# Kernel tuning notes

Hardware: AMD Instinct MI355X
Metric: run time of the kernel (lower is better)

## Reference

```python
import jax, jax.numpy as jnp
from jax import lax
import numpy as np

S, B, I, H = 1024, 512, 5, 32
G = 4 * H  # torch LSTM gate dim, order: i, f, g, o


def setup_inputs() -> dict:
    key = jax.random.key(0)
    ks = jax.random.split(key, 19)
    n = lambda k, shape, s=0.1: jax.random.normal(k, shape, jnp.float32) * s
    return {
        "x": jax.random.normal(ks[0], (S, B, I), jnp.float32),
        "Wih0": n(ks[1], (G, I)), "Whh0": n(ks[2], (G, H)), "bih0": n(ks[3], (G,)), "bhh0": n(ks[4], (G,)),
        "Wih1": n(ks[5], (G, H)), "Whh1": n(ks[6], (G, H)), "bih1": n(ks[7], (G,)), "bhh1": n(ks[8], (G,)),
        "Wih2": n(ks[9], (G, H)), "Whh2": n(ks[10], (G, H)), "bih2": n(ks[11], (G,)), "bhh2": n(ks[12], (G,)),
        "w1": n(ks[13], (H, H)), "b1": n(ks[14], (H,)),
        "w2": n(ks[15], (H, H)), "b2": n(ks[16], (H,)),
        "w3": n(ks[17], (1, H)), "b3": n(ks[18], (1,)),
    }


def lstm_layer(x, Wih, Whh, bih, bhh):
    # x: [S, B, in]; precompute input projections for all steps (one big GEMM)
    xp = jnp.einsum("sbi,gi->sbg", x, Wih) + bih + bhh  # [S, B, 4H]
    h0 = jnp.zeros((x.shape[1], H), x.dtype)
    c0 = jnp.zeros((x.shape[1], H), x.dtype)

    def step(carry, xg):
        h, c = carry
        gates = xg + h @ Whh.T  # [B, 4H]
        i, f, g, o = jnp.split(gates, 4, axis=-1)
        c = jax.nn.sigmoid(f) * c + jax.nn.sigmoid(i) * jnp.tanh(g)
        h = jax.nn.sigmoid(o) * jnp.tanh(c)
        return (h, c), h

    _, ys = lax.scan(step, (h0, c0), xp)
    return ys  # [S, B, H]


def reference(x, Wih0, Whh0, bih0, bhh0, Wih1, Whh1, bih1, bhh1,
              Wih2, Whh2, bih2, bhh2, w1, b1, w2, b2, w3, b3):
    h = lstm_layer(x, Wih0, Whh0, bih0, bhh0)
    h = lstm_layer(h, Wih1, Whh1, bih1, bhh1)
    h = lstm_layer(h, Wih2, Whh2, bih2, bhh2)  # [S, B, H]
    s, b, hd = h.shape
    y = h.reshape(s * b, hd)
    y = y @ w1.T + b1
    y = y @ w2.T + b2
    y = y @ w3.T + b3
    y = jax.nn.relu(y)
    return y.reshape(s, b, -1)  # [S, B, 1]
```

## Files before the change

kernel.cpp:

```cpp
#include <hip/hip_runtime.h>
#include <math.h>

#define S_LEN 1024
#define BATCH 512
#define HID   32

#define LOG2E 1.44269504088896340736f

__device__ __forceinline__ float fast_rcp(float x) { return __builtin_amdgcn_rcpf(x); }
__device__ __forceinline__ float fast_exp2(float x) { return __builtin_amdgcn_exp2f(x); }

__device__ __forceinline__ void tick_barrier() {
    asm volatile("s_waitcnt lgkmcnt(0)" ::: "memory");
    __builtin_amdgcn_s_barrier();
    asm volatile("" ::: "memory");
}

typedef unsigned int uint2v __attribute__((ext_vector_type(2)));
__device__ __forceinline__ void swap_halves(float v, float& hiAll, float& loAll) {
    uint2v r = __builtin_amdgcn_permlane32_swap(__float_as_uint(v),
                                                __float_as_uint(v),
                                                false, false);
    hiAll = __uint_as_float(r[0]);
    loAll = __uint_as_float(r[1]);
}

__device__ __forceinline__ float bcast(float v, int k) {
    return __int_as_float(__builtin_amdgcn_readlane(__float_as_int(v), k));
}

#define LOADROW(dst, base, row, sc)                                            \
    {                                                                          \
        const float4* W_ = reinterpret_cast<const float4*>((base) +            \
                                                    (size_t)(row) * HID);      \
        _Pragma("unroll")                                                      \
        for (int k4 = 0; k4 < 8; ++k4) {                                       \
            float4 v_ = W_[k4];                                                \
            dst[4 * k4 + 0] = v_.x * (sc);                                     \
            dst[4 * k4 + 1] = v_.y * (sc);                                     \
            dst[4 * k4 + 2] = v_.z * (sc);                                     \
            dst[4 * k4 + 3] = v_.w * (sc);                                     \
        }                                                                      \
    }

__global__ __launch_bounds__(192)
__attribute__((amdgpu_waves_per_eu(1, 2)))
void lstm3_fused(const float* __restrict__ x,
                 const float* __restrict__ Wih0, const float* __restrict__ Whh0,
                 const float* __restrict__ bih0, const float* __restrict__ bhh0,
                 const float* __restrict__ Wih1, const float* __restrict__ Whh1,
                 const float* __restrict__ bih1, const float* __restrict__ bhh1,
                 const float* __restrict__ Wih2, const float* __restrict__ Whh2,
                 const float* __restrict__ bih2, const float* __restrict__ bhh2,
                 float* __restrict__ hseq)
{
    const int b = blockIdx.x;
    const int w = threadIdx.x >> 6;
    const int l = threadIdx.x & 63;
    const int j = l & 31;
    const bool lowHalf = (l < 32);
    const int gA = l;
    const int gB = l + 64;
    const float sA = LOG2E;
    const float sB = lowHalf ? (2.0f * LOG2E) : LOG2E;

    __shared__ float4 xl4[S_LEN];
    __shared__ float  xl1[S_LEN];
    __shared__ float ring[2][2][HID];

    for (int i = threadIdx.x; i < 2 * 2 * HID; i += 192)
        (&ring[0][0][0])[i] = 0.0f;
    {
        float* xf = reinterpret_cast<float*>(xl4);
        for (int idx = threadIdx.x; idx < S_LEN * 5; idx += 192) {
            const int s = idx / 5;
            const int c = idx - 5 * s;
            const float v = x[(size_t)s * (BATCH * 5) + b * 5 + c];
            if (c < 4) xf[s * 4 + c] = v;
            else       xl1[s] = v;
        }
    }

    const float* Wih = (w == 0) ? Wih0 : (w == 1) ? Wih1 : Wih2;
    const float* Whh = (w == 0) ? Whh0 : (w == 1) ? Whh1 : Whh2;
    const float* bih = (w == 0) ? bih0 : (w == 1) ? bih1 : bih2;
    const float* bhh = (w == 0) ? bhh0 : (w == 1) ? bhh1 : bhh2;

    float whA[HID], whB[HID];
    LOADROW(whA, Whh, gA, sA);
    LOADROW(whB, Whh, gB, sB);
    float wiA[HID], wiB[HID];
    float wxA[5], wxB[5];
    if (w == 0) {
#pragma unroll
        for (int k = 0; k < 5; ++k) {
            wxA[k] = Wih[gA * 5 + k] * sA;
            wxB[k] = Wih[gB * 5 + k] * sB;
        }
    } else {
        LOADROW(wiA, Wih, gA, sA);
        LOADROW(wiB, Wih, gB, sB);
    }
    const float biasA = (bih[gA] + bhh[gA]) * sA;
    const float biasB = (bih[gB] + bhh[gB]) * sB;

    float c = 0.0f;
    float h_own = 0.0f;

    __syncthreads();

    for (int t = 0; t < S_LEN + 2; ++t) {
        const int s = t - w;
        const bool active = (s >= 0) && (s < S_LEN);
        const int p = t & 1;

        float aA0 = biasA, aA1 = 0.f, aA2 = 0.f, aA3 = 0.f;
        float aB0 = biasB, aB1 = 0.f, aB2 = 0.f, aB3 = 0.f;

#pragma unroll
        for (int k4 = 0; k4 < HID / 4; ++k4) {
            const float h0 = bcast(h_own, 4 * k4 + 0);
            const float h1 = bcast(h_own, 4 * k4 + 1);
            const float h2 = bcast(h_own, 4 * k4 + 2);
            const float h3 = bcast(h_own, 4 * k4 + 3);
            aA0 += whA[4 * k4 + 0] * h0;
            aA1 += whA[4 * k4 + 1] * h1;
            aA2 += whA[4 * k4 + 2] * h2;
            aA3 += whA[4 * k4 + 3] * h3;
            aB0 += whB[4 * k4 + 0] * h0;
            aB1 += whB[4 * k4 + 1] * h1;
            aB2 += whB[4 * k4 + 2] * h2;
            aB3 += whB[4 * k4 + 3] * h3;
        }

        if (w == 0) {
            if (active) {
                const float4 xv = xl4[s];
                const float  x4 = xl1[s];
                aA0 += wxA[0] * xv.x; aB0 += wxB[0] * xv.x;
                aA1 += wxA[1] * xv.y; aB1 += wxB[1] * xv.y;
                aA2 += wxA[2] * xv.z; aB2 += wxB[2] * xv.z;
                aA3 += wxA[3] * xv.w; aB3 += wxB[3] * xv.w;
                aA0 += wxA[4] * x4;   aB0 += wxB[4] * x4;
            }
        } else {
            const float4* hin4 = reinterpret_cast<const float4*>(&ring[p][w - 1][0]);
#pragma unroll
            for (int k4 = 0; k4 < HID / 4; ++k4) {
                float4 hv = hin4[k4];
                aA0 += wiA[4 * k4 + 0] * hv.x;
                aA1 += wiA[4 * k4 + 1] * hv.y;
                aA2 += wiA[4 * k4 + 2] * hv.z;
                aA3 += wiA[4 * k4 + 3] * hv.w;
                aB0 += wiB[4 * k4 + 0] * hv.x;
                aB1 += wiB[4 * k4 + 1] * hv.y;
                aB2 += wiB[4 * k4 + 2] * hv.z;
                aB3 += wiB[4 * k4 + 3] * hv.w;
            }
        }
        const float accA = (aA0 + aA1) + (aA2 + aA3);
        const float accB = (aB0 + aB1) + (aB2 + aB3);

        float yf, yi, yo, yg;
        swap_halves(accA, yf, yi);
        swap_halves(accB, yo, yg);

        const float gi = fast_rcp(1.0f + fast_exp2(-yi));
        const float gf = fast_rcp(1.0f + fast_exp2(-yf));
        const float sg = fast_rcp(1.0f + fast_exp2(-yg));
        const float go = fast_rcp(1.0f + fast_exp2(-yo));
        const float gg = 2.0f * sg - 1.0f;

        const float c_new = gf * c + gi * gg;
        const float e  = fast_exp2(-2.0f * LOG2E * fabsf(c_new));
        const float tc = copysignf((1.0f - e) * fast_rcp(1.0f + e), c_new);
        const float h = go * tc;

        if (active) {
            c = c_new;
            h_own = h;
            if (w < 2) {
                if (lowHalf) ring[p ^ 1][w][j] = h;
            } else {
                if (lowHalf)
                    hseq[((size_t)s * BATCH + b) * HID + j] = h;
            }
        }
        tick_barrier();
    }
}

__global__ __launch_bounds__(256)
void mlp_kernel(const float* __restrict__ h, const float* __restrict__ w1,
                const float* __restrict__ b1, const float* __restrict__ w2,
                const float* __restrict__ b2, const float* __restrict__ w3,
                const float* __restrict__ b3, float* __restrict__ out)
{
    __shared__ float W1[HID * HID];
    __shared__ float W2[HID * HID];
    __shared__ float W3[HID];
    __shared__ float B1[HID];
    __shared__ float B2[HID];
    __shared__ float B3s;

    for (int i = threadIdx.x; i < HID * HID; i += blockDim.x) {
        W1[i] = w1[i];
        W2[i] = w2[i];
    }
    if (threadIdx.x < HID) {
        W3[threadIdx.x] = w3[threadIdx.x];
        B1[threadIdx.x] = b1[threadIdx.x];
        B2[threadIdx.x] = b2[threadIdx.x];
    }
    if (threadIdx.x == 0) B3s = b3[0];
    __syncthreads();

    const size_t e = (size_t)blockIdx.x * blockDim.x + threadIdx.x;
    float hv[HID];
    const float4* hp = reinterpret_cast<const float4*>(h + e * HID);
#pragma unroll
    for (int k4 = 0; k4 < HID / 4; ++k4) {
        float4 v = hp[k4];
        hv[4 * k4 + 0] = v.x;
        hv[4 * k4 + 1] = v.y;
        hv[4 * k4 + 2] = v.z;
        hv[4 * k4 + 3] = v.w;
    }

    float y1[HID];
#pragma unroll
    for (int jj = 0; jj < HID; ++jj) {
        float acc = B1[jj];
#pragma unroll
        for (int k = 0; k < HID; ++k) acc += W1[jj * HID + k] * hv[k];
        y1[jj] = acc;
    }
    float y2[HID];
#pragma unroll
    for (int jj = 0; jj < HID; ++jj) {
        float acc = B2[jj];
#pragma unroll
        for (int k = 0; k < HID; ++k) acc += W2[jj * HID + k] * y1[k];
        y2[jj] = acc;
    }
    float acc3 = B3s;
#pragma unroll
    for (int k = 0; k < HID; ++k) acc3 += W3[k] * y2[k];
    out[e] = fmaxf(acc3, 0.0f);
}

extern "C" void kernel_launch(void* const* d_in, const int* in_sizes, int n_in,
                              void* d_out, int out_size, void* d_ws, size_t ws_size,
                              hipStream_t stream)
{
    const float* x    = (const float*)d_in[0];
    const float* Wih0 = (const float*)d_in[1];
    const float* Whh0 = (const float*)d_in[2];
    const float* bih0 = (const float*)d_in[3];
    const float* bhh0 = (const float*)d_in[4];
    const float* Wih1 = (const float*)d_in[5];
    const float* Whh1 = (const float*)d_in[6];
    const float* bih1 = (const float*)d_in[7];
    const float* bhh1 = (const float*)d_in[8];
    const float* Wih2 = (const float*)d_in[9];
    const float* Whh2 = (const float*)d_in[10];
    const float* bih2 = (const float*)d_in[11];
    const float* bhh2 = (const float*)d_in[12];
    const float* w1   = (const float*)d_in[13];
    const float* b1   = (const float*)d_in[14];
    const float* w2   = (const float*)d_in[15];
    const float* b2   = (const float*)d_in[16];
    const float* w3   = (const float*)d_in[17];
    const float* b3   = (const float*)d_in[18];

    float* hseq = (float*)d_ws;

    lstm3_fused<<<BATCH, 192, 0, stream>>>(x, Wih0, Whh0, bih0, bhh0,
                                           Wih1, Whh1, bih1, bhh1,
                                           Wih2, Whh2, bih2, bhh2, hseq);

    mlp_kernel<<<(S_LEN * BATCH) / 256, 256, 0, stream>>>(hseq, w1, b1, w2, b2, w3, b3,
                                                          (float*)d_out);
}
```

Before: 888.4 us.

## Process two batch elements per block to reuse register-resident weights

Each block now handles two batch columns instead of one, so the recurrent and input weight rows held in registers serve two independent LSTM chains, and the launch uses half as many blocks. The two chains interleave inside each timestep, which gives more instruction-level parallelism per wave and halves the number of per-step barriers counted across the whole grid. The costs are twice the LDS for the staged inputs and ring buffers, more accumulator registers, and only 256 blocks, which may underfill the GPU and lengthen the serial path each block walks.

```diff
diff --git a/kernel.cpp b/kernel.cpp
--- a/kernel.cpp
+++ b/kernel.cpp
@@ -4,6 +4,7 @@
 #define S_LEN 1024
 #define BATCH 512
 #define HID   32
+#define BPB   2
 
 #define LOG2E 1.44269504088896340736f
 
@@ -54,7 +55,7 @@
                  const float* __restrict__ bih2, const float* __restrict__ bhh2,
                  float* __restrict__ hseq)
 {
-    const int b = blockIdx.x;
+    const int b0 = blockIdx.x * BPB;
     const int w = threadIdx.x >> 6;
     const int l = threadIdx.x & 63;
     const int j = l & 31;
@@ -64,20 +65,21 @@
     const float sA = LOG2E;
     const float sB = lowHalf ? (2.0f * LOG2E) : LOG2E;
 
-    __shared__ float4 xl4[S_LEN];
-    __shared__ float  xl1[S_LEN];
-    __shared__ float ring[2][2][HID];
-
-    for (int i = threadIdx.x; i < 2 * 2 * HID; i += 192)
-        (&ring[0][0][0])[i] = 0.0f;
+    __shared__ float4 xl4[BPB][S_LEN];
+    __shared__ float  xl1[BPB][S_LEN];
+    __shared__ float ring[2][2][BPB][HID];
+
+    for (int i = threadIdx.x; i < 2 * 2 * BPB * HID; i += 192)
+        (&ring[0][0][0][0])[i] = 0.0f;
     {
-        float* xf = reinterpret_cast<float*>(xl4);
-        for (int idx = threadIdx.x; idx < S_LEN * 5; idx += 192) {
-            const int s = idx / 5;
-            const int c = idx - 5 * s;
-            const float v = x[(size_t)s * (BATCH * 5) + b * 5 + c];
-            if (c < 4) xf[s * 4 + c] = v;
-            else       xl1[s] = v;
+        for (int idx = threadIdx.x; idx < BPB * S_LEN * 5; idx += 192) {
+            const int bb = idx / (S_LEN * 5);
+            const int r  = idx - bb * (S_LEN * 5);
+            const int s  = r / 5;
+            const int c  = r - 5 * s;
+            const float v = x[(size_t)s * (BATCH * 5) + (b0 + bb) * 5 + c];
+            if (c < 4) reinterpret_cast<float*>(&xl4[bb][0])[s * 4 + c] = v;
+            else       xl1[bb][s] = v;
         }
     }
 
@@ -104,8 +106,8 @@
     const float biasA = (bih[gA] + bhh[gA]) * sA;
     const float biasB = (bih[gB] + bhh[gB]) * sB;
 
-    float c = 0.0f;
-    float h_own = 0.0f;
+    float cst[BPB]  = {0.0f, 0.0f};
+    float hown[BPB] = {0.0f, 0.0f};
 
     __syncthreads();
 
@@ -114,76 +116,93 @@
         const bool active = (s >= 0) && (s < S_LEN);
         const int p = t & 1;
 
-        float aA0 = biasA, aA1 = 0.f, aA2 = 0.f, aA3 = 0.f;
-        float aB0 = biasB, aB1 = 0.f, aB2 = 0.f, aB3 = 0.f;
+        float aA[BPB][4], aB[BPB][4];
+#pragma unroll
+        for (int bb = 0; bb < BPB; ++bb) {
+            aA[bb][0] = biasA; aA[bb][1] = 0.f; aA[bb][2] = 0.f; aA[bb][3] = 0.f;
+            aB[bb][0] = biasB; aB[bb][1] = 0.f; aB[bb][2] = 0.f; aB[bb][3] = 0.f;
+        }
 
 #pragma unroll
         for (int k4 = 0; k4 < HID / 4; ++k4) {
-            const float h0 = bcast(h_own, 4 * k4 + 0);
-            const float h1 = bcast(h_own, 4 * k4 + 1);
-            const float h2 = bcast(h_own, 4 * k4 + 2);
-            const float h3 = bcast(h_own, 4 * k4 + 3);
-            aA0 += whA[4 * k4 + 0] * h0;
-            aA1 += whA[4 * k4 + 1] * h1;
-            aA2 += whA[4 * k4 + 2] * h2;
-            aA3 += whA[4 * k4 + 3] * h3;
-            aB0 += whB[4 * k4 + 0] * h0;
-            aB1 += whB[4 * k4 + 1] * h1;
-            aB2 += whB[4 * k4 + 2] * h2;
-            aB3 += whB[4 * k4 + 3] * h3;
+#pragma unroll
+            for (int bb = 0; bb < BPB; ++bb) {
+                const float h0 = bcast(hown[bb], 4 * k4 + 0);
+                const float h1 = bcast(hown[bb], 4 * k4 + 1);
+                const float h2 = bcast(hown[bb], 4 * k4 + 2);
+                const float h3 = bcast(hown[bb], 4 * k4 + 3);
+                aA[bb][0] += whA[4 * k4 + 0] * h0;
+                aA[bb][1] += whA[4 * k4 + 1] * h1;
+                aA[bb][2] += whA[4 * k4 + 2] * h2;
+                aA[bb][3] += whA[4 * k4 + 3] * h3;
+                aB[bb][0] += whB[4 * k4 + 0] * h0;
+                aB[bb][1] += whB[4 * k4 + 1] * h1;
+                aB[bb][2] += whB[4 * k4 + 2] * h2;
+                aB[bb][3] += whB[4 * k4 + 3] * h3;
+            }
         }
 
         if (w == 0) {
             if (active) {
-                const float4 xv = xl4[s];
-                const float  x4 = xl1[s];
-                aA0 += wxA[0] * xv.x; aB0 += wxB[0] * xv.x;
-                aA1 += wxA[1] * xv.y; aB1 += wxB[1] * xv.y;
-                aA2 += wxA[2] * xv.z; aB2 += wxB[2] * xv.z;
-                aA3 += wxA[3] * xv.w; aB3 += wxB[3] * xv.w;
-                aA0 += wxA[4] * x4;   aB0 += wxB[4] * x4;
+#pragma unroll
+                for (int bb = 0; bb < BPB; ++bb) {
+                    const float4 xv = xl4[bb][s];
+                    const float  x4 = xl1[bb][s];
+                    aA[bb][0] += wxA[0] * xv.x; aB[bb][0] += wxB[0] * xv.x;
+                    aA[bb][1] += wxA[1] * xv.y; aB[bb][1] += wxB[1] * xv.y;
+                    aA[bb][2] += wxA[2] * xv.z; aB[bb][2] += wxB[2] * xv.z;
+                    aA[bb][3] += wxA[3] * xv.w; aB[bb][3] += wxB[3] * xv.w;
+                    aA[bb][0] += wxA[4] * x4;   aB[bb][0] += wxB[4] * x4;
+                }
             }
         } else {
-            const float4* hin4 = reinterpret_cast<const float4*>(&ring[p][w - 1][0]);
 #pragma unroll
             for (int k4 = 0; k4 < HID / 4; ++k4) {
-                float4 hv = hin4[k4];
-                aA0 += wiA[4 * k4 + 0] * hv.x;
-                aA1 += wiA[4 * k4 + 1] * hv.y;
-                aA2 += wiA[4 * k4 + 2] * hv.z;
-                aA3 += wiA[4 * k4 + 3] * hv.w;
-                aB0 += wiB[4 * k4 + 0] * hv.x;
-                aB1 += wiB[4 * k4 + 1] * hv.y;
-                aB2 += wiB[4 * k4 + 2] * hv.z;
-                aB3 += wiB[4 * k4 + 3] * hv.w;
+#pragma unroll
+                for (int bb = 0; bb < BPB; ++bb) {
+                    const float4 hv = reinterpret_cast<const float4*>(
+                                          &ring[p][w - 1][bb][0])[k4];
+                    aA[bb][0] += wiA[4 * k4 + 0] * hv.x;
+                    aA[bb][1] += wiA[4 * k4 + 1] * hv.y;
+                    aA[bb][2] += wiA[4 * k4 + 2] * hv.z;
+                    aA[bb][3] += wiA[4 * k4 + 3] * hv.w;
+                    aB[bb][0] += wiB[4 * k4 + 0] * hv.x;
+                    aB[bb][1] += wiB[4 * k4 + 1] * hv.y;
+                    aB[bb][2] += wiB[4 * k4 + 2] * hv.z;
+                    aB[bb][3] += wiB[4 * k4 + 3] * hv.w;
+                }
             }
         }
-        const float accA = (aA0 + aA1) + (aA2 + aA3);
-        const float accB = (aB0 + aB1) + (aB2 + aB3);
-
-        float yf, yi, yo, yg;
-        swap_halves(accA, yf, yi);
-        swap_halves(accB, yo, yg);
-
-        const float gi = fast_rcp(1.0f + fast_exp2(-yi));
-        const float gf = fast_rcp(1.0f + fast_exp2(-yf));
-        const float sg = fast_rcp(1.0f + fast_exp2(-yg));
-        const float go = fast_rcp(1.0f + fast_exp2(-yo));
-        const float gg = 2.0f * sg - 1.0f;
-
-        const float c_new = gf * c + gi * gg;
-        const float e  = fast_exp2(-2.0f * LOG2E * fabsf(c_new));
-        const float tc = copysignf((1.0f - e) * fast_rcp(1.0f + e), c_new);
-        const float h = go * tc;
-
-        if (active) {
-            c = c_new;
-            h_own = h;
-            if (w < 2) {
-                if (lowHalf) ring[p ^ 1][w][j] = h;
-            } else {
-                if (lowHalf)
-                    hseq[((size_t)s * BATCH + b) * HID + j] = h;
+
+#pragma unroll
+        for (int bb = 0; bb < BPB; ++bb) {
+            const float accA = (aA[bb][0] + aA[bb][1]) + (aA[bb][2] + aA[bb][3]);
+            const float accB = (aB[bb][0] + aB[bb][1]) + (aB[bb][2] + aB[bb][3]);
+
+            float yf, yi, yo, yg;
+            swap_halves(accA, yf, yi);
+            swap_halves(accB, yo, yg);
+
+            const float gi = fast_rcp(1.0f + fast_exp2(-yi));
+            const float gf = fast_rcp(1.0f + fast_exp2(-yf));
+            const float sg = fast_rcp(1.0f + fast_exp2(-yg));
+            const float go = fast_rcp(1.0f + fast_exp2(-yo));
+            const float gg = 2.0f * sg - 1.0f;
+
+            const float c_new = gf * cst[bb] + gi * gg;
+            const float e  = fast_exp2(-2.0f * LOG2E * fabsf(c_new));
+            const float tc = copysignf((1.0f - e) * fast_rcp(1.0f + e), c_new);
+            const float h = go * tc;
+
+            if (active) {
+                cst[bb] = c_new;
+                hown[bb] = h;
+                if (w < 2) {
+                    if (lowHalf) ring[p ^ 1][w][bb][j] = h;
+                } else {
+                    if (lowHalf)
+                        hseq[((size_t)s * BATCH + (b0 + bb)) * HID + j] = h;
+                }
             }
         }
         tick_barrier();
@@ -275,9 +294,9 @@
 
     float* hseq = (float*)d_ws;
 
-    lstm3_fused<<<BATCH, 192, 0, stream>>>(x, Wih0, Whh0, bih0, bhh0,
-                                           Wih1, Whh1, bih1, bhh1,
-                                           Wih2, Whh2, bih2, bhh2, hseq);
+    lstm3_fused<<<BATCH / BPB, 192, 0, stream>>>(x, Wih0, Whh0, bih0, bhh0,
+                                                 Wih1, Whh1, bih1, bhh1,
+                                                 Wih2, Whh2, bih2, bhh2, hseq);
 
     mlp_kernel<<<(S_LEN * BATCH) / 256, 256, 0, stream>>>(hseq, w1, b1, w2, b2, w3, b3,
                                                           (float*)d_out);
```

Result: slower. 1.209 ms (+36.0%).

## Fuse collapsed linear MLP head into LSTM kernel and halve barrier count

Applied to the files above, without the earlier changes.

The three linear layers are folded into a single 32-vector dot product plus a scalar bias, since there is no nonlinearity before the final ReLU. Each block computes this once, and wave 2 reduces h·v with lane shuffles and writes the output directly. This drops the hseq workspace write and the separate MLP launch. The layer skew is widened to 2 steps with a 4-slot ring, so the barrier now runs once every two timesteps. The waves_per_eu attribute is also removed. Risks are a small floating-point reassociation difference from collapsing the MLP, and a longer pipeline fill.

```diff
diff --git a/kernel.cpp b/kernel.cpp
--- a/kernel.cpp
+++ b/kernel.cpp
@@ -44,7 +44,6 @@
     }
 
 __global__ __launch_bounds__(192)
-__attribute__((amdgpu_waves_per_eu(1, 2)))
 void lstm3_fused(const float* __restrict__ x,
                  const float* __restrict__ Wih0, const float* __restrict__ Whh0,
                  const float* __restrict__ bih0, const float* __restrict__ bhh0,
@@ -52,7 +51,10 @@
                  const float* __restrict__ bih1, const float* __restrict__ bhh1,
                  const float* __restrict__ Wih2, const float* __restrict__ Whh2,
                  const float* __restrict__ bih2, const float* __restrict__ bhh2,
-                 float* __restrict__ hseq)
+                 const float* __restrict__ w1, const float* __restrict__ b1,
+                 const float* __restrict__ w2, const float* __restrict__ b2,
+                 const float* __restrict__ w3, const float* __restrict__ b3,
+                 float* __restrict__ out)
 {
     const int b = blockIdx.x;
     const int w = threadIdx.x >> 6;
@@ -66,9 +68,9 @@
 
     __shared__ float4 xl4[S_LEN];
     __shared__ float  xl1[S_LEN];
-    __shared__ float ring[2][2][HID];
-
-    for (int i = threadIdx.x; i < 2 * 2 * HID; i += 192)
+    __shared__ float ring[4][2][HID];
+
+    for (int i = threadIdx.x; i < 4 * 2 * HID; i += 192)
         (&ring[0][0][0])[i] = 0.0f;
     {
         float* xf = reinterpret_cast<float*>(xl4);
@@ -104,149 +106,123 @@
     const float biasA = (bih[gA] + bhh[gA]) * sA;
     const float biasB = (bih[gB] + bhh[gB]) * sB;
 
+    float v_j = 0.0f, cbias = 0.0f;
+    if (w == 2) {
+        float uacc[HID];
+#pragma unroll
+        for (int k = 0; k < HID; ++k) uacc[k] = 0.0f;
+        for (int r = 0; r < HID; ++r) {
+            const float w3r = w3[r];
+#pragma unroll
+            for (int k = 0; k < HID; ++k)
+                uacc[k] += w3r * w2[r * HID + k];
+        }
+#pragma unroll
+        for (int k = 0; k < HID; ++k) {
+            v_j  += uacc[k] * w1[k * HID + j];
+            cbias += uacc[k] * b1[k];
+        }
+        for (int r = 0; r < HID; ++r) cbias += w3[r] * b2[r];
+        cbias += b3[0];
+    }
+
     float c = 0.0f;
     float h_own = 0.0f;
 
     __syncthreads();
 
-    for (int t = 0; t < S_LEN + 2; ++t) {
-        const int s = t - w;
-        const bool active = (s >= 0) && (s < S_LEN);
-        const int p = t & 1;
-
-        float aA0 = biasA, aA1 = 0.f, aA2 = 0.f, aA3 = 0.f;
-        float aB0 = biasB, aB1 = 0.f, aB2 = 0.f, aB3 = 0.f;
-
-#pragma unroll
-        for (int k4 = 0; k4 < HID / 4; ++k4) {
-            const float h0 = bcast(h_own, 4 * k4 + 0);
-            const float h1 = bcast(h_own, 4 * k4 + 1);
-            const float h2 = bcast(h_own, 4 * k4 + 2);
-            const float h3 = bcast(h_own, 4 * k4 + 3);
-            aA0 += whA[4 * k4 + 0] * h0;
-            aA1 += whA[4 * k4 + 1] * h1;
-            aA2 += whA[4 * k4 + 2] * h2;
-            aA3 += whA[4 * k4 + 3] * h3;
-            aB0 += whB[4 * k4 + 0] * h0;
-            aB1 += whB[4 * k4 + 1] * h1;
-            aB2 += whB[4 * k4 + 2] * h2;
-            aB3 += whB[4 * k4 + 3] * h3;
-        }
-
-        if (w == 0) {
+    for (int t = 0; t < S_LEN + 4; t += 2) {
+#pragma unroll
+        for (int u = 0; u < 2; ++u) {
+            const int tt = t + u;
+            const int s = tt - 2 * w;
+            const bool active = (s >= 0) && (s < S_LEN);
+            const int wslot = tt & 3;
+            const int rslot = wslot ^ 2;
+
+            float aA0 = biasA, aA1 = 0.f, aA2 = 0.f, aA3 = 0.f;
+            float aB0 = biasB, aB1 = 0.f, aB2 = 0.f, aB3 = 0.f;
+
+#pragma unroll
+            for (int k4 = 0; k4 < HID / 4; ++k4) {
+                const float h0 = bcast(h_own, 4 * k4 + 0);
+                const float h1 = bcast(h_own, 4 * k4 + 1);
+                const float h2 = bcast(h_own, 4 * k4 + 2);
+                const float h3 = bcast(h_own, 4 * k4 + 3);
+                aA0 += whA[4 * k4 + 0] * h0;
+                aA1 += whA[4 * k4 + 1] * h1;
+                aA2 += whA[4 * k4 + 2] * h2;
+                aA3 += whA[4 * k4 + 3] * h3;
+                aB0 += whB[4 * k4 + 0] * h0;
+                aB1 += whB[4 * k4 + 1] * h1;
+                aB2 += whB[4 * k4 + 2] * h2;
+                aB3 += whB[4 * k4 + 3] * h3;
+            }
+
+            if (w == 0) {
+                if (active) {
+                    const float4 xv = xl4[s];
+                    const float  x4 = xl1[s];
+                    aA0 += wxA[0] * xv.x; aB0 += wxB[0] * xv.x;
+                    aA1 += wxA[1] * xv.y; aB1 += wxB[1] * xv.y;
+                    aA2 += wxA[2] * xv.z; aB2 += wxB[2] * xv.z;
+                    aA3 += wxA[3] * xv.w; aB3 += wxB[3] * xv.w;
+                    aA0 += wxA[4] * x4;   aB0 += wxB[4] * x4;
+                }
+            } else {
+                const float4* hin4 =
+                    reinterpret_cast<const float4*>(&ring[rslot][w - 1][0]);
+#pragma unroll
+                for (int k4 = 0; k4 < HID / 4; ++k4) {
+                    float4 hv = hin4[k4];
+                    aA0 += wiA[4 * k4 + 0] * hv.x;
+                    aA1 += wiA[4 * k4 + 1] * hv.y;
+                    aA2 += wiA[4 * k4 + 2] * hv.z;
+                    aA3 += wiA[4 * k4 + 3] * hv.w;
+                    aB0 += wiB[4 * k4 + 0] * hv.x;
+                    aB1 += wiB[4 * k4 + 1] * hv.y;
+                    aB2 += wiB[4 * k4 + 2] * hv.z;
+                    aB3 += wiB[4 * k4 + 3] * hv.w;
+                }
+            }
+            const float accA = (aA0 + aA1) + (aA2 + aA3);
+            const float accB = (aB0 + aB1) + (aB2 + aB3);
+
+            float yf, yi, yo, yg;
+            swap_halves(accA, yf, yi);
+            swap_halves(accB, yo, yg);
+
+            const float gi = fast_rcp(1.0f + fast_exp2(-yi));
+            const float gf = fast_rcp(1.0f + fast_exp2(-yf));
+            const float sg = fast_rcp(1.0f + fast_exp2(-yg));
+            const float go = fast_rcp(1.0f + fast_exp2(-yo));
+            const float gg = 2.0f * sg - 1.0f;
+
+            const float c_new = gf * c + gi * gg;
+            const float e  = fast_exp2(-2.0f * LOG2E * fabsf(c_new));
+            const float tc = copysignf((1.0f - e) * fast_rcp(1.0f + e), c_new);
+            const float h = go * tc;
+
             if (active) {
-                const float4 xv = xl4[s];
-                const float  x4 = xl1[s];
-                aA0 += wxA[0] * xv.x; aB0 += wxB[0] * xv.x;
-                aA1 += wxA[1] * xv.y; aB1 += wxB[1] * xv.y;
-                aA2 += wxA[2] * xv.z; aB2 += wxB[2] * xv.z;
-                aA3 += wxA[3] * xv.w; aB3 += wxB[3] * xv.w;
-                aA0 += wxA[4] * x4;   aB0 += wxB[4] * x4;
+                c = c_new;
+                h_own = h;
+                if (w < 2) {
+                    if (lowHalf) ring[wslot][w][j] = h;
+                } else {
+                    float prod = h * v_j;
+                    prod += __shfl_xor(prod, 16);
+                    prod += __shfl_xor(prod, 8);
+                    prod += __shfl_xor(prod, 4);
+                    prod += __shfl_xor(prod, 2);
+                    prod += __shfl_xor(prod, 1);
+                    const float y = fmaxf(prod + cbias, 0.0f);
+                    if (l == 0)
+                        out[(size_t)s * BATCH + b] = y;
+                }
             }
-        } else {
-            const float4* hin4 = reinterpret_cast<const float4*>(&ring[p][w - 1][0]);
-#pragma unroll
-            for (int k4 = 0; k4 < HID / 4; ++k4) {
-                float4 hv = hin4[k4];
-                aA0 += wiA[4 * k4 + 0] * hv.x;
-                aA1 += wiA[4 * k4 + 1] * hv.y;
-                aA2 += wiA[4 * k4 + 2] * hv.z;
-                aA3 += wiA[4 * k4 + 3] * hv.w;
-                aB0 += wiB[4 * k4 + 0] * hv.x;
-                aB1 += wiB[4 * k4 + 1] * hv.y;
-                aB2 += wiB[4 * k4 + 2] * hv.z;
-                aB3 += wiB[4 * k4 + 3] * hv.w;
-            }
-        }
-        const float accA = (aA0 + aA1) + (aA2 + aA3);
-        const float accB = (aB0 + aB1) + (aB2 + aB3);
-
-        float yf, yi, yo, yg;
-        swap_halves(accA, yf, yi);
-        swap_halves(accB, yo, yg);
-
-        const float gi = fast_rcp(1.0f + fast_exp2(-yi));
-        const float gf = fast_rcp(1.0f + fast_exp2(-yf));
-        const float sg = fast_rcp(1.0f + fast_exp2(-yg));
-        const float go = fast_rcp(1.0f + fast_exp2(-yo));
-        const float gg = 2.0f * sg - 1.0f;
-
-        const float c_new = gf * c + gi * gg;
-        const float e  = fast_exp2(-2.0f * LOG2E * fabsf(c_new));
-        const float tc = copysignf((1.0f - e) * fast_rcp(1.0f + e), c_new);
-        const float h = go * tc;
-
-        if (active) {
-            c = c_new;
-            h_own = h;
-            if (w < 2) {
-                if (lowHalf) ring[p ^ 1][w][j] = h;
-            } else {
-                if (lowHalf)
-                    hseq[((size_t)s * BATCH + b) * HID + j] = h;
-            }
         }
         tick_barrier();
     }
-}
-
-__global__ __launch_bounds__(256)
-void mlp_kernel(const float* __restrict__ h, const float* __restrict__ w1,
-                const float* __restrict__ b1, const float* __restrict__ w2,
-                const float* __restrict__ b2, const float* __restrict__ w3,
-                const float* __restrict__ b3, float* __restrict__ out)
-{
-    __shared__ float W1[HID * HID];
-    __shared__ float W2[HID * HID];
-    __shared__ float W3[HID];
-    __shared__ float B1[HID];
-    __shared__ float B2[HID];
-    __shared__ float B3s;
-
-    for (int i = threadIdx.x; i < HID * HID; i += blockDim.x) {
-        W1[i] = w1[i];
-        W2[i] = w2[i];
-    }
-    if (threadIdx.x < HID) {
-        W3[threadIdx.x] = w3[threadIdx.x];
-        B1[threadIdx.x] = b1[threadIdx.x];
-        B2[threadIdx.x] = b2[threadIdx.x];
-    }
-    if (threadIdx.x == 0) B3s = b3[0];
-    __syncthreads();
-
-    const size_t e = (size_t)blockIdx.x * blockDim.x + threadIdx.x;
-    float hv[HID];
-    const float4* hp = reinterpret_cast<const float4*>(h + e * HID);
-#pragma unroll
-    for (int k4 = 0; k4 < HID / 4; ++k4) {
-        float4 v = hp[k4];
-        hv[4 * k4 + 0] = v.x;
-        hv[4 * k4 + 1] = v.y;
-        hv[4 * k4 + 2] = v.z;
-        hv[4 * k4 + 3] = v.w;
-    }
-
-    float y1[HID];
-#pragma unroll
-    for (int jj = 0; jj < HID; ++jj) {
-        float acc = B1[jj];
-#pragma unroll
-        for (int k = 0; k < HID; ++k) acc += W1[jj * HID + k] * hv[k];
-        y1[jj] = acc;
-    }
-    float y2[HID];
-#pragma unroll
-    for (int jj = 0; jj < HID; ++jj) {
-        float acc = B2[jj];
-#pragma unroll
-        for (int k = 0; k < HID; ++k) acc += W2[jj * HID + k] * y1[k];
-        y2[jj] = acc;
-    }
-    float acc3 = B3s;
-#pragma unroll
-    for (int k = 0; k < HID; ++k) acc3 += W3[k] * y2[k];
-    out[e] = fmaxf(acc3, 0.0f);
 }
 
 extern "C" void kernel_launch(void* const* d_in, const int* in_sizes, int n_in,
@@ -273,12 +249,9 @@
     const float* w3   = (const float*)d_in[17];
     const float* b3   = (const float*)d_in[18];
 
-    float* hseq = (float*)d_ws;
-
     lstm3_fused<<<BATCH, 192, 0, stream>>>(x, Wih0, Whh0, bih0, bhh0,
                                            Wih1, Whh1, bih1, bhh1,
-                                           Wih2, Whh2, bih2, bhh2, hseq);
-
-    mlp_kernel<<<(S_LEN * BATCH) / 256, 256, 0, stream>>>(hseq, w1, b1, w2, b2, w3, b3,
-                                                          (float*)d_out);
-}
+                                           Wih2, Whh2, bih2, bhh2,
+                                           w1, b1, w2, b2, w3, b3,
+                                           (float*)d_out);
+}
```

Result: slower. 1.422 ms (+60.1%).
